# Kernel optimization log

Hardware: AMD Instinct MI355X
Metric: run time of the kernel (lower is better)

The kernel has to match this reference:

```python
import jax, jax.numpy as jnp
import numpy as np

B, T, F_IN, L, D = 512, 32, 4096, 256, 256
EPS = 1e-8
KM_ITERS = 100


def _linear(x, w, b):
    return x @ w.T + b


def _clf(h, w0, b0, w1, b1, w2, b2, w3, b3):
    # Linear->ReLU (Dropout is identity in eval) x3 then final Linear
    h = jax.nn.relu(_linear(h, w0, b0))
    h = jax.nn.relu(_linear(h, w1, b1))
    h = jax.nn.relu(_linear(h, w2, b2))
    return _linear(h, w3, b3)


def _kmeans_cosine(f):
    # f: (T, L). 2-cluster kmeans with cosine distance, fixed iteration count.
    fn = f / (jnp.linalg.norm(f, axis=1, keepdims=True) + EPS)
    centers0 = jnp.stack([f[0], f[T // 2]])  # deterministic init (ref: random pick)

    def step(centers, _):
        cn = centers / (jnp.linalg.norm(centers, axis=1, keepdims=True) + EPS)
        sim = fn @ cn.T                           # (T,2) cosine similarity
        assign = jnp.argmax(sim, axis=1)          # argmin of (1 - sim)
        mask = jax.nn.one_hot(assign, 2, dtype=f.dtype)  # (T,2)
        counts = mask.sum(axis=0)                 # (2,)
        new = (mask.T @ f) / jnp.clip(counts, 1.0)[:, None]
        new = jnp.where(counts[:, None] > 0, new, centers)
        return new, assign

    centers, assigns = jax.lax.scan(step, centers0, None, length=KM_ITERS)
    return assigns[-1], centers


def setup_inputs() -> dict:
    key = jax.random.key(0)
    ks = jax.random.split(key, 32)
    s = 0.02
    inp = {
        "x": jax.random.normal(ks[0], (B, T, F_IN), dtype=jnp.float32),
        "tsn_w": jax.random.normal(ks[1], (L, F_IN, 3), dtype=jnp.float32) * s,
        "tsn_b": jnp.zeros((L,), jnp.float32),
        "aV_w": jax.random.normal(ks[2], (D, L), dtype=jnp.float32) * s,
        "aV_b": jnp.zeros((D,), jnp.float32),
        "aU_w": jax.random.normal(ks[3], (D, L), dtype=jnp.float32) * s,
        "aU_b": jnp.zeros((D,), jnp.float32),
        "gate_w": jax.random.normal(ks[4], (1, D), dtype=jnp.float32) * s,
        "gate_b": jnp.zeros((1,), jnp.float32),
    }
    dims_bag = [(D, L), (D // 2, D), (32, D // 2), (1, 32)]
    dims_seg = [(D, L + 1), (D // 2, D), (32, D // 2), (1, 32)]
    for j, (o, i) in enumerate(dims_bag):
        inp[f"cb_w{j}"] = jax.random.normal(ks[5 + j], (o, i), dtype=jnp.float32) * s
        inp[f"cb_b{j}"] = jnp.zeros((o,), jnp.float32)
    for j, (o, i) in enumerate(dims_seg):
        inp[f"cs_w{j}"] = jax.random.normal(ks[9 + j], (o, i), dtype=jnp.float32) * s
        inp[f"cs_b{j}"] = jnp.zeros((o,), jnp.float32)
    return inp


def reference(x, tsn_w, tsn_b, aV_w, aV_b, aU_w, aU_b, gate_w, gate_b,
              cb_w0, cb_b0, cb_w1, cb_b1, cb_w2, cb_b2, cb_w3, cb_b3,
              cs_w0, cs_b0, cs_w1, cs_b1, cs_w2, cs_b2, cs_w3, cs_b3):
    feat_in = jnp.nan_to_num(x)  # (B,T,4096)
    # Conv1d over time (kernel 3, pad 1): NCH layout
    feature = jax.lax.conv_general_dilated(
        feat_in.transpose(0, 2, 1), tsn_w, (1,), [(1, 1)],
        dimension_numbers=('NCH', 'OIH', 'NCH')) + tsn_b[None, :, None]
    feature = feature.transpose(0, 2, 1)  # (B,T,L)

    # Gated MIL attention
    A_V = jnp.tanh(_linear(feature, aV_w, aV_b))
    A_U = jax.nn.sigmoid(_linear(feature, aU_w, aU_b))
    A = _linear(A_V * A_U, gate_w, gate_b)      # (B,T,1)
    At = A.transpose(0, 2, 1)                   # (B,1,T)
    bag = jnp.einsum('bot,btl->bol', jax.nn.softmax(At, axis=2), feature)[:, 0]  # (B,L)

    output1 = jax.nn.sigmoid(_clf(bag, cb_w0, cb_b0, cb_w1, cb_b1,
                                  cb_w2, cb_b2, cb_w3, cb_b3)).reshape(-1)  # (B,)

    seg_in = jnp.concatenate([feature, A], axis=2)  # (B,T,L+1)
    output_seg = jax.nn.sigmoid(_clf(seg_in, cs_w0, cs_b0, cs_w1, cs_b1,
                                     cs_w2, cs_b2, cs_w3, cs_b3)[..., 0])  # (B,T)

    # Per-sample 2-means cosine clustering (batched via vmap instead of python loop)
    assigns, _ = jax.vmap(_kmeans_cosine)(feature)  # (B,T) int
    mask0 = assigns == 0
    cnt0 = mask0.sum(1).astype(output_seg.dtype)
    cnt1 = T - cnt0
    m0 = jnp.where(mask0, output_seg, 0.0).sum(1) / jnp.clip(cnt0, 1.0)
    m1 = jnp.where(~mask0, output_seg, 0.0).sum(1) / jnp.clip(cnt1, 1.0)
    m0 = jnp.where(cnt0 > 0, m0, -jnp.inf)
    m1 = jnp.where(cnt1 > 0, m1, -jnp.inf)
    output2 = jnp.maximum(m0, m1)  # (B,)

    weight = 0.5
    output = jnp.stack([output1 * weight, output2 * (1.0 - weight)], axis=1)  # (B,2)
    # (ragged cluster index lists replaced by the dense assignment map `assigns`)
    return feature, assigns, output_seg, output, At
```

## Files before the change

kernel.cpp:

```cpp
#include <hip/hip_runtime.h>
#include <cfloat>
#include <cmath>

#define NB 512
#define NT 32
#define FIN 4096
#define NL 256
#define ND 256
#define NM (NB*NT)
#define KCONV (3*FIN)
#define PLANE 3145728

#define BM 128
#define BN 128
#define BK 32
#define LDT 132

typedef __attribute__((ext_vector_type(8))) short short8_t;
typedef __attribute__((ext_vector_type(4))) float f32x4;

__device__ __forceinline__ float sigmoidf_(float v) { return 1.0f / (1.0f + expf(-v)); }

__device__ __forceinline__ unsigned short f2bf(float v) {
  unsigned u = __float_as_uint(v);
  unsigned r = u + 0x7FFFu + ((u >> 16) & 1u);
  return (unsigned short)(r >> 16);
}
__device__ __forceinline__ float bf2f(unsigned short h) {
  return __uint_as_float(((unsigned)h) << 16);
}

__global__ void __launch_bounds__(256) repack_frag_k(const float* __restrict__ w,
                                                     unsigned short* __restrict__ wt) {
  int d = blockIdx.x * 256 + threadIdx.x;
  int kt = d >> 13;
  int bc = (d >> 9) & 15;
  int lane = (d >> 3) & 63;
  int j = d & 7;
  int kb = lane >> 4;
  int kk = kt * 32 + kb * 8 + j;
  int l = bc * 16 + (lane & 15);
  int tap = kk >> 12;
  int f = kk & 4095;
  float v = w[(size_t)l * KCONV + f * 3 + tap];
  unsigned short hi = f2bf(v);
  unsigned short lo = f2bf(v - bf2f(hi));
  wt[d] = hi;
  wt[PLANE + d] = lo;
}

__global__ void __launch_bounds__(256) repack_dense_k(const float* __restrict__ W1,
    const float* __restrict__ W2, int nsplit, int ldw, int KB, int N16,
    unsigned short* __restrict__ wt, int planeElems) {
  int d = blockIdx.x * 256 + threadIdx.x;
  if (d >= planeElems) return;
  int j = d & 7;
  int lane = (d >> 3) & 63;
  int bckt = d >> 9;
  int bc = bckt % N16;
  int kt = bckt / N16;
  int kk = kt * 32 + (lane >> 4) * 8 + j;
  int l = bc * 16 + (lane & 15);
  float v = 0.f;
  if (kk < KB) {
    if (l < nsplit) v = W1[(size_t)l * ldw + kk];
    else            v = W2[(size_t)(l - nsplit) * ldw + kk];
  }
  unsigned short hi = f2bf(v);
  unsigned short lo = f2bf(v - bf2f(hi));
  wt[d] = hi;
  wt[planeElems + d] = lo;
}

__global__ void __launch_bounds__(256) conv_mfma_k(const float* __restrict__ x,
    const unsigned short* __restrict__ WT, float* __restrict__ PART) {
  __shared__ __align__(16) unsigned short AS[8192];
  __shared__ __align__(16) unsigned short BS[8192];
  const int tid = threadIdx.x;
  const int m0 = blockIdx.x * 128;
  const int by = blockIdx.y;
  const int ktBase = blockIdx.z * 192;
  const int lane = tid & 63;
  const int w = tid >> 6, wr = w >> 1, wc = w & 1;
  const int kb = tid & 3;
  const int rquot = tid >> 2;

  f32x4 acc[4][4] = {};
  float4 avreg[4];
  short8_t bvreg[4];

  {
    int ktg = ktBase;
    int tap = ktg >> 7;
    int f0 = (ktg & 127) << 5;
#pragma unroll
    for (int u = 0; u < 2; ++u) {
      int row = u * 64 + rquot;
      int gm = m0 + row;
      int tt = (gm & 31) + tap - 1;
      if ((unsigned)tt < 32u) {
        const float* src = x + (size_t)(gm + tap - 1) * FIN + f0 + kb * 8;
        avreg[u*2+0] = *reinterpret_cast<const float4*>(src);
        avreg[u*2+1] = *reinterpret_cast<const float4*>(src + 4);
      } else {
        avreg[u*2+0] = make_float4(0,0,0,0);
        avreg[u*2+1] = make_float4(0,0,0,0);
      }
    }
    const unsigned short* bsrc = WT + ((size_t)ktg * 16 + by * 8) * 512;
#pragma unroll
    for (int q = 0; q < 4; ++q) {
      int p = q >> 1, pass = q & 1;
      bvreg[q] = *reinterpret_cast<const short8_t*>(bsrc + (size_t)p * PLANE + (pass*256 + tid) * 8);
    }
  }

  for (int i = 0; i < 192; ++i) {
#pragma unroll
    for (int u = 0; u < 2; ++u) {
      float vv[8];
      *reinterpret_cast<float4*>(&vv[0]) = avreg[u*2+0];
      *reinterpret_cast<float4*>(&vv[4]) = avreg[u*2+1];
      __align__(16) unsigned short hi[8];
      __align__(16) unsigned short lo[8];
#pragma unroll
      for (int e = 0; e < 8; ++e) {
        float v = vv[e];
        v = (v == v) ? v : 0.0f;
        unsigned short h = f2bf(v);
        hi[e] = h;
        lo[e] = f2bf(v - bf2f(h));
      }
      int row = u * 64 + rquot;
      int br = row >> 4;
      int lanew = (row & 15) + (kb << 4);
      int off = br * 512 + lanew * 8;
      *reinterpret_cast<short8_t*>(AS + off)        = *reinterpret_cast<const short8_t*>(hi);
      *reinterpret_cast<short8_t*>(AS + 4096 + off) = *reinterpret_cast<const short8_t*>(lo);
    }
#pragma unroll
    for (int q = 0; q < 4; ++q) {
      int p = q >> 1, pass = q & 1;
      *reinterpret_cast<short8_t*>(BS + p * 4096 + (pass*256 + tid) * 8) = bvreg[q];
    }
    __syncthreads();

    if (i + 1 < 192) {
      int ktg = ktBase + i + 1;
      int tap = ktg >> 7;
      int f0 = (ktg & 127) << 5;
#pragma unroll
      for (int u = 0; u < 2; ++u) {
        int row = u * 64 + rquot;
        int gm = m0 + row;
        int tt = (gm & 31) + tap - 1;
        if ((unsigned)tt < 32u) {
          const float* src = x + (size_t)(gm + tap - 1) * FIN + f0 + kb * 8;
          avreg[u*2+0] = *reinterpret_cast<const float4*>(src);
          avreg[u*2+1] = *reinterpret_cast<const float4*>(src + 4);
        } else {
          avreg[u*2+0] = make_float4(0,0,0,0);
          avreg[u*2+1] = make_float4(0,0,0,0);
        }
      }
      const unsigned short* bsrc = WT + ((size_t)ktg * 16 + by * 8) * 512;
#pragma unroll
      for (int q = 0; q < 4; ++q) {
        int p = q >> 1, pass = q & 1;
        bvreg[q] = *reinterpret_cast<const short8_t*>(bsrc + (size_t)p * PLANE + (pass*256 + tid) * 8);
      }
    }

    short8_t bh[4], bl[4];
#pragma unroll
    for (int c = 0; c < 4; ++c) {
      int bc = wc * 4 + c;
      bh[c] = *reinterpret_cast<const short8_t*>(BS + bc * 512 + lane * 8);
      bl[c] = *reinterpret_cast<const short8_t*>(BS + 4096 + bc * 512 + lane * 8);
    }
#pragma unroll
    for (int r = 0; r < 4; ++r) {
      int br = wr * 4 + r;
      short8_t ah = *reinterpret_cast<const short8_t*>(AS + br * 512 + lane * 8);
      short8_t al = *reinterpret_cast<const short8_t*>(AS + 4096 + br * 512 + lane * 8);
#pragma unroll
      for (int c = 0; c < 4; ++c) {
        acc[r][c] = __builtin_amdgcn_mfma_f32_16x16x32_bf16(ah, bh[c], acc[r][c], 0, 0, 0);
        acc[r][c] = __builtin_amdgcn_mfma_f32_16x16x32_bf16(ah, bl[c], acc[r][c], 0, 0, 0);
        acc[r][c] = __builtin_amdgcn_mfma_f32_16x16x32_bf16(al, bh[c], acc[r][c], 0, 0, 0);
      }
    }
    __syncthreads();
  }

  float* P = PART + (size_t)blockIdx.z * ((size_t)NM * NL);
#pragma unroll
  for (int r = 0; r < 4; ++r) {
#pragma unroll
    for (int c = 0; c < 4; ++c) {
#pragma unroll
      for (int e = 0; e < 4; ++e) {
        int row = m0 + wr * 64 + r * 16 + ((lane >> 4) << 2) + e;
        int col = by * 128 + wc * 64 + c * 16 + (lane & 15);
        P[(size_t)row * NL + col] = acc[r][c][e];
      }
    }
  }
}

__global__ void __launch_bounds__(256) reduce_bias_k(const float* __restrict__ PART,
    const float* __restrict__ bias, float* __restrict__ feat) {
  int i = blockIdx.x * 256 + threadIdx.x;
  size_t base = (size_t)i * 4;
  float4 a = *reinterpret_cast<const float4*>(PART + base);
  float4 b = *reinterpret_cast<const float4*>(PART + (size_t)NM * NL + base);
  int c0 = (int)(base & 255);
  float4 bb = *reinterpret_cast<const float4*>(bias + c0);
  float4 o;
  o.x = a.x + b.x + bb.x;
  o.y = a.y + b.y + bb.y;
  o.z = a.z + b.z + bb.z;
  o.w = a.w + b.w + bb.w;
  *reinterpret_cast<float4*>(feat + base) = o;
}

template <int ACT, int SEG>
__global__ void __launch_bounds__(256) mfma_gemm_k(const float* __restrict__ A, int lda,
    const float* __restrict__ Aws, const unsigned short* __restrict__ WT,
    int planeElems, int N16, int KT,
    const float* __restrict__ bias1, const float* __restrict__ bias2, int bsplit,
    float* __restrict__ C, int N) {
  __shared__ __align__(16) unsigned short AS[8192];
  __shared__ __align__(16) unsigned short BS[8192];
  const int tid = threadIdx.x;
  const int m0 = blockIdx.x * 128;
  const int by = blockIdx.y;
  const int lane = tid & 63;
  const int w = tid >> 6, wr = w >> 1, wc = w & 1;
  const int kb = tid & 3;
  const int rquot = tid >> 2;

  f32x4 acc[4][4] = {};
  float4 avreg[4];
  short8_t bvreg[4];

  {
    int kk0 = 0;
#pragma unroll
    for (int u = 0; u < 2; ++u) {
      int gm = m0 + u * 64 + rquot;
      const float* src = A + (size_t)gm * lda + kk0 + kb * 8;
      avreg[u*2+0] = *reinterpret_cast<const float4*>(src);
      avreg[u*2+1] = *reinterpret_cast<const float4*>(src + 4);
    }
    const unsigned short* bsrc = WT + ((size_t)(0 * N16) + by * 8) * 512;
#pragma unroll
    for (int q = 0; q < 4; ++q) {
      int p = q >> 1, pass = q & 1;
      bvreg[q] = *reinterpret_cast<const short8_t*>(bsrc + (size_t)p * planeElems * 8 / 8
                  + (size_t)p * 0 + (pass*256 + tid) * 8 + (size_t)(p ? planeElems - planeElems : 0));
    }
#pragma unroll
    for (int q = 0; q < 4; ++q) {
      int p = q >> 1, pass = q & 1;
      bvreg[q] = *reinterpret_cast<const short8_t*>(WT + (size_t)p * planeElems
                  + ((size_t)by * 8) * 512 + (pass*256 + tid) * 8);
    }
  }

  for (int i = 0; i < KT; ++i) {
#pragma unroll
    for (int u = 0; u < 2; ++u) {
      float vv[8];
      *reinterpret_cast<float4*>(&vv[0]) = avreg[u*2+0];
      *reinterpret_cast<float4*>(&vv[4]) = avreg[u*2+1];
      __align__(16) unsigned short hi[8];
      __align__(16) unsigned short lo[8];
#pragma unroll
      for (int e = 0; e < 8; ++e) {
        float v = vv[e];
        unsigned short h = f2bf(v);
        hi[e] = h;
        lo[e] = f2bf(v - bf2f(h));
      }
      int row = u * 64 + rquot;
      int br = row >> 4;
      int lanew = (row & 15) + (kb << 4);
      int off = br * 512 + lanew * 8;
      *reinterpret_cast<short8_t*>(AS + off)        = *reinterpret_cast<const short8_t*>(hi);
      *reinterpret_cast<short8_t*>(AS + 4096 + off) = *reinterpret_cast<const short8_t*>(lo);
    }
#pragma unroll
    for (int q = 0; q < 4; ++q) {
      int p = q >> 1, pass = q & 1;
      *reinterpret_cast<short8_t*>(BS + p * 4096 + (pass*256 + tid) * 8) = bvreg[q];
    }
    __syncthreads();

    if (i + 1 < KT) {
      int kk0 = (i + 1) * 32;
#pragma unroll
      for (int u = 0; u < 2; ++u) {
        int gm = m0 + u * 64 + rquot;
        if (SEG && kk0 >= 256) {
          float a0 = (kb == 0) ? Aws[gm] : 0.f;
          avreg[u*2+0] = make_float4(a0, 0.f, 0.f, 0.f);
          avreg[u*2+1] = make_float4(0.f, 0.f, 0.f, 0.f);
        } else {
          const float* src = A + (size_t)gm * lda + kk0 + kb * 8;
          avreg[u*2+0] = *reinterpret_cast<const float4*>(src);
          avreg[u*2+1] = *reinterpret_cast<const float4*>(src + 4);
        }
      }
#pragma unroll
      for (int q = 0; q < 4; ++q) {
        int p = q >> 1, pass = q & 1;
        bvreg[q] = *reinterpret_cast<const short8_t*>(WT + (size_t)p * planeElems
                    + ((size_t)(i + 1) * N16 + by * 8) * 512 + (pass*256 + tid) * 8);
      }
    }

    short8_t bh[4], bl[4];
#pragma unroll
    for (int c = 0; c < 4; ++c) {
      int bc = wc * 4 + c;
      bh[c] = *reinterpret_cast<const short8_t*>(BS + bc * 512 + lane * 8);
      bl[c] = *reinterpret_cast<const short8_t*>(BS + 4096 + bc * 512 + lane * 8);
    }
#pragma unroll
    for (int r = 0; r < 4; ++r) {
      int br = wr * 4 + r;
      short8_t ah = *reinterpret_cast<const short8_t*>(AS + br * 512 + lane * 8);
      short8_t al = *reinterpret_cast<const short8_t*>(AS + 4096 + br * 512 + lane * 8);
#pragma unroll
      for (int c = 0; c < 4; ++c) {
        acc[r][c] = __builtin_amdgcn_mfma_f32_16x16x32_bf16(ah, bh[c], acc[r][c], 0, 0, 0);
        acc[r][c] = __builtin_amdgcn_mfma_f32_16x16x32_bf16(ah, bl[c], acc[r][c], 0, 0, 0);
        acc[r][c] = __builtin_amdgcn_mfma_f32_16x16x32_bf16(al, bh[c], acc[r][c], 0, 0, 0);
      }
    }
    __syncthreads();
  }

#pragma unroll
  for (int r = 0; r < 4; ++r) {
#pragma unroll
    for (int c = 0; c < 4; ++c) {
#pragma unroll
      for (int e = 0; e < 4; ++e) {
        int row = m0 + wr * 64 + r * 16 + ((lane >> 4) << 2) + e;
        int col = by * 128 + wc * 64 + c * 16 + (lane & 15);
        float b = (col < bsplit) ? bias1[col] : bias2[col - bsplit];
        float v = acc[r][c][e] + b;
        if (ACT == 1) v = fmaxf(v, 0.f);
        C[(size_t)row * N + col] = v;
      }
    }
  }
}

template <int ACT>
__global__ void __launch_bounds__(256) gemm_wt_k(const float* __restrict__ A, int lda,
    const float* __restrict__ W, int ldw, int KB,
    const float* __restrict__ bias, float* __restrict__ C,
    int N, int K) {
  __shared__ float As[BK][LDT];
  __shared__ float Bs[BK][LDT];
  const int tid = threadIdx.x;
  const int m0 = blockIdx.x * BM;
  const int n0 = blockIdx.y * BN;
  const int row0 = (tid >> 4) << 3;
  const int col0 = (tid & 15) << 3;
  float acc[8][8] = {};
  for (int kk0 = 0; kk0 < K; kk0 += BK) {
#pragma unroll
    for (int i = 0; i < 4; ++i) {
      int v = i * 256 + tid;
      int row = v >> 3;
      int f4 = (v & 7) << 2;
      float4 val = *reinterpret_cast<const float4*>(A + (size_t)(m0 + row) * lda + kk0 + f4);
      As[f4 + 0][row] = val.x;
      As[f4 + 1][row] = val.y;
      As[f4 + 2][row] = val.z;
      As[f4 + 3][row] = val.w;
    }
#pragma unroll
    for (int i = 0; i < 4; ++i) {
      int v = i * 256 + tid;
      int n = v >> 3;
      int kq = (v & 7) << 2;
      int gn = n0 + n;
#pragma unroll
      for (int j = 0; j < 4; ++j) {
        int kk = kk0 + kq + j;
        float bv = 0.f;
        if (gn < N && kk < KB) bv = W[(size_t)gn * ldw + kk];
        Bs[kq + j][n] = bv;
      }
    }
    __syncthreads();
#pragma unroll
    for (int kk = 0; kk < BK; ++kk) {
      float a[8], b[8];
      *reinterpret_cast<float4*>(&a[0]) = *reinterpret_cast<const float4*>(&As[kk][row0]);
      *reinterpret_cast<float4*>(&a[4]) = *reinterpret_cast<const float4*>(&As[kk][row0 + 4]);
      *reinterpret_cast<float4*>(&b[0]) = *reinterpret_cast<const float4*>(&Bs[kk][col0]);
      *reinterpret_cast<float4*>(&b[4]) = *reinterpret_cast<const float4*>(&Bs[kk][col0 + 4]);
#pragma unroll
      for (int r = 0; r < 8; ++r)
#pragma unroll
        for (int c = 0; c < 8; ++c)
          acc[r][c] = fmaf(a[r], b[c], acc[r][c]);
    }
    __syncthreads();
  }
#pragma unroll
  for (int r = 0; r < 8; ++r) {
    int m = m0 + row0 + r;
#pragma unroll
    for (int c = 0; c < 8; ++c) {
      int n = n0 + col0 + c;
      if (n < N) {
        float v = acc[r][c] + bias[n];
        if (ACT == 1) v = fmaxf(v, 0.f);
        C[(size_t)m * (size_t)N + n] = v;
      }
    }
  }
}

__global__ void __launch_bounds__(256) gate_k(const float* __restrict__ Y,
    const float* __restrict__ gw, const float* __restrict__ gb,
    float* __restrict__ Aws, float* __restrict__ At) {
  int lane = threadIdx.x & 63;
  int m = blockIdx.x * 4 + (threadIdx.x >> 6);
  float4 v4 = *reinterpret_cast<const float4*>(Y + (size_t)m * 512 + lane * 4);
  float4 u4 = *reinterpret_cast<const float4*>(Y + (size_t)m * 512 + 256 + lane * 4);
  float4 g4 = *reinterpret_cast<const float4*>(gw + lane * 4);
  float s = tanhf(v4.x) * sigmoidf_(u4.x) * g4.x
          + tanhf(v4.y) * sigmoidf_(u4.y) * g4.y
          + tanhf(v4.z) * sigmoidf_(u4.z) * g4.z
          + tanhf(v4.w) * sigmoidf_(u4.w) * g4.w;
#pragma unroll
  for (int off = 32; off > 0; off >>= 1) s += __shfl_xor(s, off, 64);
  if (lane == 0) {
    float a = s + gb[0];
    Aws[m] = a;
    At[m] = a;
  }
}

__global__ void __launch_bounds__(256) softmax_bag_k(const float* __restrict__ Aws,
    const float* __restrict__ feat, float* __restrict__ bag) {
  __shared__ float av[NT];
  __shared__ float ev[NT];
  int b = blockIdx.x, tid = threadIdx.x;
  if (tid < NT) av[tid] = Aws[b * NT + tid];
  __syncthreads();
  float mx = -FLT_MAX;
#pragma unroll
  for (int t = 0; t < NT; ++t) mx = fmaxf(mx, av[t]);
  if (tid < NT) ev[tid] = expf(av[tid] - mx);
  __syncthreads();
  float ssum = 0.f;
#pragma unroll
  for (int t = 0; t < NT; ++t) ssum += ev[t];
  float accv = 0.f;
#pragma unroll
  for (int t = 0; t < NT; ++t) accv += ev[t] * feat[((size_t)b * NT + t) * NL + tid];
  bag[(size_t)b * NL + tid] = accv / ssum;
}

__global__ void __launch_bounds__(256) rowdot32_k(const float* __restrict__ H,
    const float* __restrict__ w, const float* __restrict__ bptr,
    float* __restrict__ outp, int ostride, float scale) {
  int m = blockIdx.x * 256 + threadIdx.x;
  const float* h = H + (size_t)m * 32;
  float s = bptr[0];
#pragma unroll
  for (int i = 0; i < 32; i += 4) {
    float4 hv = *reinterpret_cast<const float4*>(h + i);
    float4 wv = *reinterpret_cast<const float4*>(w + i);
    s += hv.x * wv.x + hv.y * wv.y + hv.z * wv.z + hv.w * wv.w;
  }
  outp[(size_t)m * ostride] = scale * sigmoidf_(s);
}

__global__ void __launch_bounds__(64) kmeans_k(const float* __restrict__ feat,
    const float* __restrict__ seg, float* __restrict__ assigns_out,
    float* __restrict__ outpair) {
  __shared__ float fls[NT][260];
  int b = blockIdx.x, lane = threadIdx.x;
  int l0 = lane << 2;
  float fn[NT][4];
#pragma unroll
  for (int t = 0; t < NT; ++t) {
    float4 v = *reinterpret_cast<const float4*>(feat + ((size_t)b * NT + t) * NL + l0);
    *reinterpret_cast<float4*>(&fls[t][l0]) = v;
    float ss = v.x * v.x + v.y * v.y + v.z * v.z + v.w * v.w;
#pragma unroll
    for (int off = 32; off > 0; off >>= 1) ss += __shfl_xor(ss, off, 64);
    float nr = sqrtf(ss) + 1e-8f;
    fn[t][0] = v.x / nr; fn[t][1] = v.y / nr; fn[t][2] = v.z / nr; fn[t][3] = v.w / nr;
  }
  __syncthreads();
  float cr0[4], cr1[4];
#pragma unroll
  for (int i = 0; i < 4; ++i) { cr0[i] = fls[0][l0 + i]; cr1[i] = fls[16][l0 + i]; }

  unsigned long long amask = 0ull;
  unsigned long long prev = ~0ull;
  int c1n = 0;
  for (int it = 0; it < 100; ++it) {
    float ss0 = cr0[0]*cr0[0] + cr0[1]*cr0[1] + cr0[2]*cr0[2] + cr0[3]*cr0[3];
    float ss1 = cr1[0]*cr1[0] + cr1[1]*cr1[1] + cr1[2]*cr1[2] + cr1[3]*cr1[3];
#pragma unroll
    for (int off = 32; off > 0; off >>= 1) {
      ss0 += __shfl_xor(ss0, off, 64);
      ss1 += __shfl_xor(ss1, off, 64);
    }
    float nr0 = sqrtf(ss0) + 1e-8f, nr1 = sqrtf(ss1) + 1e-8f;
    float cn0[4], cn1[4];
#pragma unroll
    for (int i = 0; i < 4; ++i) { cn0[i] = cr0[i] / nr0; cn1[i] = cr1[i] / nr1; }
    float p[64];
#pragma unroll
    for (int t = 0; t < NT; ++t) {
      p[2*t]   = fn[t][0]*cn0[0] + fn[t][1]*cn0[1] + fn[t][2]*cn0[2] + fn[t][3]*cn0[3];
      p[2*t+1] = fn[t][0]*cn1[0] + fn[t][1]*cn1[1] + fn[t][2]*cn1[2] + fn[t][3]*cn1[3];
    }
    float v32[32];
    { bool hi = (lane & 32) != 0;
#pragma unroll
      for (int i = 0; i < 32; ++i) {
        float keep = hi ? p[32+i] : p[i];
        float send = hi ? p[i] : p[32+i];
        v32[i] = keep + __shfl_xor(send, 32, 64);
      } }
    float v16[16];
    { bool hi = (lane & 16) != 0;
#pragma unroll
      for (int i = 0; i < 16; ++i) {
        float keep = hi ? v32[16+i] : v32[i];
        float send = hi ? v32[i] : v32[16+i];
        v16[i] = keep + __shfl_xor(send, 16, 64);
      } }
    float v8[8];
    { bool hi = (lane & 8) != 0;
#pragma unroll
      for (int i = 0; i < 8; ++i) {
        float keep = hi ? v16[8+i] : v16[i];
        float send = hi ? v16[i] : v16[8+i];
        v8[i] = keep + __shfl_xor(send, 8, 64);
      } }
    float v4[4];
    { bool hi = (lane & 4) != 0;
#pragma unroll
      for (int i = 0; i < 4; ++i) {
        float keep = hi ? v8[4+i] : v8[i];
        float send = hi ? v8[i] : v8[4+i];
        v4[i] = keep + __shfl_xor(send, 4, 64);
      } }
    float v2[2];
    { bool hi = (lane & 2) != 0;
#pragma unroll
      for (int i = 0; i < 2; ++i) {
        float keep = hi ? v4[2+i] : v4[i];
        float send = hi ? v4[i] : v4[2+i];
        v2[i] = keep + __shfl_xor(send, 2, 64);
      } }
    float sim;
    { bool hi = (lane & 1) != 0;
      float keep = hi ? v2[1] : v2[0];
      float send = hi ? v2[0] : v2[1];
      sim = keep + __shfl_xor(send, 1, 64);
    }
    float simo = __shfl_xor(sim, 1, 64);
    bool is0 = (lane & 1) == 0;
    unsigned long long mask = __ballot(is0 && (simo > sim));
    int c1 = __popcll(mask);
    int c0 = NT - c1;
    amask = mask; c1n = c1;
    if (mask == prev) break;
    prev = mask;
    float s0v[4] = {0,0,0,0}, s1v[4] = {0,0,0,0};
#pragma unroll
    for (int t = 0; t < NT; ++t) {
      float mt = (float)((mask >> (2*t)) & 1ull);
      float nt = 1.0f - mt;
      float4 fv = *reinterpret_cast<const float4*>(&fls[t][l0]);
      s1v[0] = fmaf(mt, fv.x, s1v[0]); s1v[1] = fmaf(mt, fv.y, s1v[1]);
      s1v[2] = fmaf(mt, fv.z, s1v[2]); s1v[3] = fmaf(mt, fv.w, s1v[3]);
      s0v[0] = fmaf(nt, fv.x, s0v[0]); s0v[1] = fmaf(nt, fv.y, s0v[1]);
      s0v[2] = fmaf(nt, fv.z, s0v[2]); s0v[3] = fmaf(nt, fv.w, s0v[3]);
    }
    float fc0 = fmaxf((float)c0, 1.0f), fc1 = fmaxf((float)c1, 1.0f);
#pragma unroll
    for (int i = 0; i < 4; ++i) {
      float n0v = s0v[i] / fc0;
      float n1v = s1v[i] / fc1;
      cr0[i] = (c0 > 0) ? n0v : cr0[i];
      cr1[i] = (c1 > 0) ? n1v : cr1[i];
    }
  }
  if (lane < NT)
    assigns_out[(size_t)b * NT + lane] = (amask & (1ull << (2*lane))) ? 1.0f : 0.0f;
  if (lane == 0) {
    float sum0 = 0.f, sum1 = 0.f;
    for (int t = 0; t < NT; ++t) {
      float sv = seg[(size_t)b * NT + t];
      if (amask & (1ull << (2*t))) sum1 += sv; else sum0 += sv;
    }
    int c1 = c1n, c0 = NT - c1n;
    float m0 = (c0 > 0) ? (sum0 / fmaxf((float)c0, 1.f)) : -INFINITY;
    float m1 = (c1 > 0) ? (sum1 / fmaxf((float)c1, 1.f)) : -INFINITY;
    outpair[(size_t)b * 2 + 1] = 0.5f * fmaxf(m0, m1);
  }
}

extern "C" void kernel_launch(void* const* d_in, const int* in_sizes, int n_in,
                              void* d_out, int out_size, void* d_ws, size_t ws_size,
                              hipStream_t stream) {
  const float* x      = (const float*)d_in[0];
  const float* tsn_w  = (const float*)d_in[1];
  const float* tsn_b  = (const float*)d_in[2];
  const float* aV_w   = (const float*)d_in[3];
  const float* aV_b   = (const float*)d_in[4];
  const float* aU_w   = (const float*)d_in[5];
  const float* aU_b   = (const float*)d_in[6];
  const float* gate_w = (const float*)d_in[7];
  const float* gate_b = (const float*)d_in[8];
  const float* cb_w0  = (const float*)d_in[9];
  const float* cb_b0  = (const float*)d_in[10];
  const float* cb_w1  = (const float*)d_in[11];
  const float* cb_b1  = (const float*)d_in[12];
  const float* cb_w2  = (const float*)d_in[13];
  const float* cb_b2  = (const float*)d_in[14];
  const float* cb_w3  = (const float*)d_in[15];
  const float* cb_b3  = (const float*)d_in[16];
  const float* cs_w0  = (const float*)d_in[17];
  const float* cs_b0  = (const float*)d_in[18];
  const float* cs_w1  = (const float*)d_in[19];
  const float* cs_b1  = (const float*)d_in[20];
  const float* cs_w2  = (const float*)d_in[21];
  const float* cs_b2  = (const float*)d_in[22];
  const float* cs_w3  = (const float*)d_in[23];
  const float* cs_b3  = (const float*)d_in[24];

  float* out = (float*)d_out;
  float* o_feat   = out;
  float* o_assign = out + 4194304;
  float* o_seg    = out + 4210688;
  float* o_out    = out + 4227072;
  float* o_At     = out + 4228096;

  char* ws = (char*)d_ws;
  unsigned short* WT = (unsigned short*)ws;
  float* PART  = (float*)(ws + 12582912);
  unsigned short* WVU = (unsigned short*)ws;
  unsigned short* WC0 = (unsigned short*)(ws + 524288);
  unsigned short* WC1 = (unsigned short*)(ws + 819200);
  float* AWS   = (float*)(ws + 950272);
  float* BAG   = (float*)(ws + 1015808);
  float* BH0   = (float*)(ws + 1540096);
  float* BH1   = (float*)(ws + 2064384);
  float* BH2   = (float*)(ws + 2326528);
  float* Y     = (float*)(ws + 12582912);
  float* SH0   = (float*)(ws + 12582912);
  float* SH1   = (float*)(ws + 29360128);
  float* SH2   = (float*)(ws + 37748736);

  repack_frag_k<<<dim3(12288), dim3(256), 0, stream>>>(tsn_w, WT);
  conv_mfma_k<<<dim3(128, 2, 2), dim3(256), 0, stream>>>(x, WT, PART);
  reduce_bias_k<<<dim3(4096), dim3(256), 0, stream>>>(PART, tsn_b, o_feat);
  repack_dense_k<<<dim3(512), dim3(256), 0, stream>>>(aV_w, aU_w, 256, 256, 256, 32, WVU, 131072);
  repack_dense_k<<<dim3(288), dim3(256), 0, stream>>>(cs_w0, cs_w0, 256, 257, 257, 16, WC0, 73728);
  repack_dense_k<<<dim3(128), dim3(256), 0, stream>>>(cs_w1, cs_w1, 256, 256, 256, 8, WC1, 32768);
  mfma_gemm_k<0,0><<<dim3(128, 4), dim3(256), 0, stream>>>(o_feat, 256, nullptr, WVU,
      131072, 32, 8, aV_b, aU_b, 256, Y, 512);
  gate_k<<<dim3(4096), dim3(256), 0, stream>>>(Y, gate_w, gate_b, AWS, o_At);
  softmax_bag_k<<<dim3(512), dim3(256), 0, stream>>>(AWS, o_feat, BAG);
  gemm_wt_k<1><<<dim3(4, 2), dim3(256), 0, stream>>>(BAG, 256, cb_w0, 256, 256, cb_b0, BH0, 256, 256);
  gemm_wt_k<1><<<dim3(4, 1), dim3(256), 0, stream>>>(BH0, 256, cb_w1, 256, 256, cb_b1, BH1, 128, 256);
  gemm_wt_k<1><<<dim3(4, 1), dim3(256), 0, stream>>>(BH1, 128, cb_w2, 128, 128, cb_b2, BH2, 32, 128);
  rowdot32_k<<<dim3(2), dim3(256), 0, stream>>>(BH2, cb_w3, cb_b3, o_out, 2, 0.5f);
  mfma_gemm_k<1,1><<<dim3(128, 2), dim3(256), 0, stream>>>(o_feat, 256, AWS, WC0,
      73728, 16, 9, cs_b0, cs_b0, 256, SH0, 256);
  mfma_gemm_k<1,0><<<dim3(128, 1), dim3(256), 0, stream>>>(SH0, 256, nullptr, WC1,
      32768, 8, 8, cs_b1, cs_b1, 128, SH1, 128);
  gemm_wt_k<1><<<dim3(128, 1), dim3(256), 0, stream>>>(SH1, 128, cs_w2, 128, 128, cs_b2, SH2, 32, 128);
  rowdot32_k<<<dim3(64), dim3(256), 0, stream>>>(SH2, cs_w3, cs_b3, o_seg, 1, 1.0f);
  kmeans_k<<<dim3(512), dim3(64), 0, stream>>>(o_feat, o_seg, o_assign, o_out);
}
```

Measured before the change: 625.6 us.

## Swizzle A-tile LDS slots in MFMA GEMMs and derive cluster-0 sum from total

Adds an aslot() permutation for where each thread writes its bf16 A fragment in LDS and where each lane reads it, in both the conv and the generic MFMA GEMM kernels. The aim is to cut LDS bank conflicts on the 16-byte stores and loads. It also removes a dead duplicate load of the B fragments in the prologue of the generic GEMM. In the k-means kernel the per-iteration cluster-0 sum is now the precomputed total minus the cluster-1 sum, which halves the FMAs in that loop at the cost of slightly different floating-point rounding.

New measurement: 675.3 us. 7.9% more time.

```diff
diff --git a/kernel.cpp b/kernel.cpp
--- a/kernel.cpp
+++ b/kernel.cpp
@@ -28,6 +28,9 @@
 }
 __device__ __forceinline__ float bf2f(unsigned short h) {
   return __uint_as_float(((unsigned)h) << 16);
+}
+__device__ __forceinline__ int aslot(int R, int kc) {
+  return ((R + 2 * kc) & 7) + 8 * ((R >> 3) + 2 * kc);
 }
 
 __global__ void __launch_bounds__(256) repack_frag_k(const float* __restrict__ w,
@@ -84,6 +87,8 @@
   const int w = tid >> 6, wr = w >> 1, wc = w & 1;
   const int kb = tid & 3;
   const int rquot = tid >> 2;
+  const int wslot = aslot(rquot & 15, kb);
+  const int rdoff = aslot(lane & 15, lane >> 4) * 8;
 
   f32x4 acc[4][4] = {};
   float4 avreg[4];
@@ -133,8 +138,7 @@
       }
       int row = u * 64 + rquot;
       int br = row >> 4;
-      int lanew = (row & 15) + (kb << 4);
-      int off = br * 512 + lanew * 8;
+      int off = br * 512 + wslot * 8;
       *reinterpret_cast<short8_t*>(AS + off)        = *reinterpret_cast<const short8_t*>(hi);
       *reinterpret_cast<short8_t*>(AS + 4096 + off) = *reinterpret_cast<const short8_t*>(lo);
     }
@@ -181,8 +185,8 @@
 #pragma unroll
     for (int r = 0; r < 4; ++r) {
       int br = wr * 4 + r;
-      short8_t ah = *reinterpret_cast<const short8_t*>(AS + br * 512 + lane * 8);
-      short8_t al = *reinterpret_cast<const short8_t*>(AS + 4096 + br * 512 + lane * 8);
+      short8_t ah = *reinterpret_cast<const short8_t*>(AS + br * 512 + rdoff);
+      short8_t al = *reinterpret_cast<const short8_t*>(AS + 4096 + br * 512 + rdoff);
 #pragma unroll
       for (int c = 0; c < 4; ++c) {
         acc[r][c] = __builtin_amdgcn_mfma_f32_16x16x32_bf16(ah, bh[c], acc[r][c], 0, 0, 0);
@@ -239,26 +243,20 @@
   const int w = tid >> 6, wr = w >> 1, wc = w & 1;
   const int kb = tid & 3;
   const int rquot = tid >> 2;
+  const int wslot = aslot(rquot & 15, kb);
+  const int rdoff = aslot(lane & 15, lane >> 4) * 8;
 
   f32x4 acc[4][4] = {};
   float4 avreg[4];
   short8_t bvreg[4];
 
   {
-    int kk0 = 0;
 #pragma unroll
     for (int u = 0; u < 2; ++u) {
       int gm = m0 + u * 64 + rquot;
-      const float* src = A + (size_t)gm * lda + kk0 + kb * 8;
+      const float* src = A + (size_t)gm * lda + kb * 8;
       avreg[u*2+0] = *reinterpret_cast<const float4*>(src);
       avreg[u*2+1] = *reinterpret_cast<const float4*>(src + 4);
-    }
-    const unsigned short* bsrc = WT + ((size_t)(0 * N16) + by * 8) * 512;
-#pragma unroll
-    for (int q = 0; q < 4; ++q) {
-      int p = q >> 1, pass = q & 1;
-      bvreg[q] = *reinterpret_cast<const short8_t*>(bsrc + (size_t)p * planeElems * 8 / 8
-                  + (size_t)p * 0 + (pass*256 + tid) * 8 + (size_t)(p ? planeElems - planeElems : 0));
     }
 #pragma unroll
     for (int q = 0; q < 4; ++q) {
@@ -285,8 +283,7 @@
       }
       int row = u * 64 + rquot;
       int br = row >> 4;
-      int lanew = (row & 15) + (kb << 4);
-      int off = br * 512 + lanew * 8;
+      int off = br * 512 + wslot * 8;
       *reinterpret_cast<short8_t*>(AS + off)        = *reinterpret_cast<const short8_t*>(hi);
       *reinterpret_cast<short8_t*>(AS + 4096 + off) = *reinterpret_cast<const short8_t*>(lo);
     }
@@ -330,8 +327,8 @@
 #pragma unroll
     for (int r = 0; r < 4; ++r) {
       int br = wr * 4 + r;
-      short8_t ah = *reinterpret_cast<const short8_t*>(AS + br * 512 + lane * 8);
-      short8_t al = *reinterpret_cast<const short8_t*>(AS + 4096 + br * 512 + lane * 8);
+      short8_t ah = *reinterpret_cast<const short8_t*>(AS + br * 512 + rdoff);
+      short8_t al = *reinterpret_cast<const short8_t*>(AS + 4096 + br * 512 + rdoff);
 #pragma unroll
       for (int c = 0; c < 4; ++c) {
         acc[r][c] = __builtin_amdgcn_mfma_f32_16x16x32_bf16(ah, bh[c], acc[r][c], 0, 0, 0);
@@ -505,6 +502,12 @@
   }
   __syncthreads();
   float cr0[4], cr1[4];
+  float tot[4] = {0.f, 0.f, 0.f, 0.f};
+#pragma unroll
+  for (int t = 0; t < NT; ++t) {
+    float4 fv = *reinterpret_cast<const float4*>(&fls[t][l0]);
+    tot[0] += fv.x; tot[1] += fv.y; tot[2] += fv.z; tot[3] += fv.w;
+  }
 #pragma unroll
   for (int i = 0; i < 4; ++i) { cr0[i] = fls[0][l0 + i]; cr1[i] = fls[16][l0 + i]; }
 
@@ -583,21 +586,18 @@
     amask = mask; c1n = c1;
     if (mask == prev) break;
     prev = mask;
-    float s0v[4] = {0,0,0,0}, s1v[4] = {0,0,0,0};
+    float s1v[4] = {0,0,0,0};
 #pragma unroll
     for (int t = 0; t < NT; ++t) {
       float mt = (float)((mask >> (2*t)) & 1ull);
-      float nt = 1.0f - mt;
       float4 fv = *reinterpret_cast<const float4*>(&fls[t][l0]);
       s1v[0] = fmaf(mt, fv.x, s1v[0]); s1v[1] = fmaf(mt, fv.y, s1v[1]);
       s1v[2] = fmaf(mt, fv.z, s1v[2]); s1v[3] = fmaf(mt, fv.w, s1v[3]);
-      s0v[0] = fmaf(nt, fv.x, s0v[0]); s0v[1] = fmaf(nt, fv.y, s0v[1]);
-      s0v[2] = fmaf(nt, fv.z, s0v[2]); s0v[3] = fmaf(nt, fv.w, s0v[3]);
     }
     float fc0 = fmaxf((float)c0, 1.0f), fc1 = fmaxf((float)c1, 1.0f);
 #pragma unroll
     for (int i = 0; i < 4; ++i) {
-      float n0v = s0v[i] / fc0;
+      float n0v = (tot[i] - s1v[i]) / fc0;
       float n1v = s1v[i] / fc1;
       cr0[i] = (c0 > 0) ? n0v : cr0[i];
       cr1[i] = (c1 > 0) ? n1v : cr1[i];
```
